# Kernel tuning notes

Measured on AMD Instinct MI355X. Metric: run time of the kernel, lower is better.

## Reference

```python
import jax, jax.numpy as jnp
import numpy as np
from jax import lax

DN = ('NHWC', 'HWIO', 'NHWC')
N_MEM = 2000  # memory slots
BN_EPS = 1e-3


def _conv(x, w, b):
    # tf.nn.conv2d stride 2, SAME, NHWC / HWIO
    return lax.conv_general_dilated(x, w, (2, 2), 'SAME', dimension_numbers=DN) + b


def _convt(x, w, b):
    # tf.nn.conv2d_transpose; w is TF layout [kh, kw, out_ch, in_ch]
    return lax.conv_transpose(x, w, (2, 2), 'SAME', dimension_numbers=DN,
                              transpose_kernel=True) + b


def _bn(x, g, b):
    # BatchNormalization(training=True): batch statistics over N,H,W
    m = jnp.mean(x, axis=(0, 1, 2))
    v = jnp.var(x, axis=(0, 1, 2))
    return g * (x - m) * lax.rsqrt(v + BN_EPS) + b


def setup_inputs() -> dict:
    key = jax.random.key(0)
    ks = iter(jax.random.split(key, 40))
    def gn(shape, s=0.05):
        return jax.random.normal(next(ks), shape, jnp.float32) * s
    inp = {'x': jax.random.uniform(next(ks), (16, 256, 256, 3), jnp.float32)}
    inp.update(
        w_e1=gn((1, 1, 3, 16)), b_e1=gn((16,)),
        g_bn1=jnp.ones(16, jnp.float32), be_bn1=jnp.zeros(16, jnp.float32),
        w_e2=gn((3, 3, 16, 32)), b_e2=gn((32,)),
        g_bn2=jnp.ones(32, jnp.float32), be_bn2=jnp.zeros(32, jnp.float32),
        w_e3=gn((3, 3, 32, 64)), b_e3=gn((64,)),
        g_bn3=jnp.ones(64, jnp.float32), be_bn3=jnp.zeros(64, jnp.float32),
        w_mem=gn((1, 1, N_MEM, 64)),
        w_d1=gn((3, 3, 32, 64)), b_d1=gn((32,)),
        g_bnt1=jnp.ones(32, jnp.float32), be_bnt1=jnp.zeros(32, jnp.float32),
        w_d2=gn((3, 3, 16, 32)), b_d2=gn((16,)),
        g_bnt2=jnp.ones(16, jnp.float32), be_bnt2=jnp.zeros(16, jnp.float32),
        w_d3=gn((3, 3, 3, 16)), b_d3=gn((3,)),
    )
    return inp


def reference(x, w_e1, b_e1, g_bn1, be_bn1, w_e2, b_e2, g_bn2, be_bn2,
              w_e3, b_e3, g_bn3, be_bn3, w_mem,
              w_d1, b_d1, g_bnt1, be_bnt1, w_d2, b_d2, g_bnt2, be_bnt2,
              w_d3, b_d3):
    # ---- encode ----
    h = jax.nn.relu(_bn(_conv(x, w_e1, b_e1), g_bn1, be_bn1))   # [B,128,128,16]
    h = jax.nn.relu(_bn(_conv(h, w_e2, b_e2), g_bn2, be_bn2))   # [B,64,64,32]
    z = jax.nn.relu(_bn(_conv(h, w_e3, b_e3), g_bn3, be_bn3))   # [B,32,32,64]
    # ---- memory addressing ----
    mem = w_mem[0, 0]                                            # [N, 64]
    num = jnp.einsum('bhwc,nc->bhwn', z, mem)
    den = jnp.einsum('bhwc,nc->bhwn', z * z, mem * mem)
    att = jax.nn.softmax((num + 1e-12) / (den + 1e-12), axis=-1)  # [B,32,32,N]
    d = att - 1.0 / N_MEM                                        # hard shrinkage
    renorm = jnp.clip(jax.nn.relu(d) * att / (jnp.abs(d) + 1e-12),
                      1e-12, 1.0 - 1e-12)
    z_hat = jnp.einsum('bhwn,nc->bhwc', renorm, mem)             # [B,32,32,64]
    # ---- decode ----
    t = jax.nn.relu(_bn(_convt(z_hat, w_d1, b_d1), g_bnt1, be_bnt1))  # [B,64,64,32]
    t = jax.nn.relu(_bn(_convt(t, w_d2, b_d2), g_bnt2, be_bnt2))      # [B,128,128,16]
    x_hat = jnp.clip(_convt(t, w_d3, b_d3), 1e-12, 1.0 - 1e-12)       # [B,256,256,3]
    return x_hat
```

## Files before the change

kernel.cpp:

```cpp
#include <hip/hip_runtime.h>
#include <math.h>

typedef __bf16 bf16x8 __attribute__((ext_vector_type(8)));
typedef __bf16 bf16x4 __attribute__((ext_vector_type(4)));
typedef float  f32x16 __attribute__((ext_vector_type(16)));

static __device__ __forceinline__ f32x16 zero16() {
  f32x16 v;
  #pragma unroll
  for (int i = 0; i < 16; ++i) v[i] = 0.f;
  return v;
}
static __device__ __forceinline__ unsigned int bfbits(__bf16 b) {
  return (unsigned int)__builtin_bit_cast(unsigned short, b);
}
static __device__ __forceinline__ bf16x8 mk8(unsigned int a, unsigned int b,
                                             unsigned int c, unsigned int d) {
  uint4 t; t.x = a; t.y = b; t.z = c; t.w = d;
  return __builtin_bit_cast(bf16x8, t);
}

__global__ __launch_bounds__(256) void k_conv1(const float* __restrict__ x,
    const float* __restrict__ w, const float* __restrict__ b, float* __restrict__ y,
    float* __restrict__ partials) {
  int t = blockIdx.x*256 + threadIdx.x;
  int ox = t & 127, oy = (t >> 7) & 127, bb = t >> 14;
  const float* xp = x + ((size_t)((bb*256 + 2*oy)*256 + 2*ox))*3;
  float x0 = xp[0], x1 = xp[1], x2 = xp[2];
  float4 rg[4];
  float4* yp = (float4*)(y + (size_t)t*16);
  #pragma unroll
  for (int g = 0; g < 4; ++g) {
    float4 r;
    r.x = b[g*4+0] + x0*w[g*4+0] + x1*w[16+g*4+0] + x2*w[32+g*4+0];
    r.y = b[g*4+1] + x0*w[g*4+1] + x1*w[16+g*4+1] + x2*w[32+g*4+1];
    r.z = b[g*4+2] + x0*w[g*4+2] + x1*w[16+g*4+2] + x2*w[32+g*4+2];
    r.w = b[g*4+3] + x0*w[g*4+3] + x1*w[16+g*4+3] + x2*w[32+g*4+3];
    rg[g] = r;
    yp[g] = r;
  }
  float4 s4[4], q4[4];
  #pragma unroll
  for (int g=0; g<4; ++g) {
    s4[g] = rg[g];
    q4[g] = make_float4(rg[g].x*rg[g].x, rg[g].y*rg[g].y, rg[g].z*rg[g].z, rg[g].w*rg[g].w);
  }
  #pragma unroll
  for (int off=1; off<64; off<<=1) {
    #pragma unroll
    for (int g=0; g<4; ++g) {
      s4[g].x += __shfl_xor(s4[g].x, off); s4[g].y += __shfl_xor(s4[g].y, off);
      s4[g].z += __shfl_xor(s4[g].z, off); s4[g].w += __shfl_xor(s4[g].w, off);
      q4[g].x += __shfl_xor(q4[g].x, off); q4[g].y += __shfl_xor(q4[g].y, off);
      q4[g].z += __shfl_xor(q4[g].z, off); q4[g].w += __shfl_xor(q4[g].w, off);
    }
  }
  __shared__ float red[4][32];
  int wv = threadIdx.x >> 6, lane = threadIdx.x & 63;
  if (lane == 0) {
    #pragma unroll
    for (int g=0; g<4; ++g) {
      *(float4*)&red[wv][g*4]      = s4[g];
      *(float4*)&red[wv][16 + g*4] = q4[g];
    }
  }
  __syncthreads();
  if (threadIdx.x < 32)
    partials[(size_t)blockIdx.x*32 + threadIdx.x] =
      red[0][threadIdx.x]+red[1][threadIdx.x]+red[2][threadIdx.x]+red[3][threadIdx.x];
}

template<int C,int CSPLIT>
__global__ __launch_bounds__(256) void k_finalize2(const float* __restrict__ partials, int nblk,
    double inv_n, const float* __restrict__ g, const float* __restrict__ be, float* __restrict__ ss) {
  const int COUTT = C/CSPLIT;
  const int NSTAT = 2*C;
  const int PER = 256/NSTAT;
  __shared__ double red[256];
  int tid = threadIdx.x;
  int st = tid % NSTAT, sub = tid / NSTAT;
  int c = st % C, kind = st / C;
  int cq = c / COUTT, j = c % COUTT;
  int nb = nblk / CSPLIT;
  double acc = 0.0;
  #pragma unroll 4
  for (int i = sub; i < nb; i += PER) {
    int bq = cq + i*CSPLIT;
    acc += (double)partials[(size_t)bq*2*COUTT + kind*COUTT + j];
  }
  red[tid] = acc;
  __syncthreads();
  for (int off = PER>>1; off > 0; off >>= 1) {
    if (sub < off) red[tid] += red[tid + off*NSTAT];
    __syncthreads();
  }
  if (tid < C) {
    double mean = red[tid]*inv_n;
    double var  = red[C+tid]*inv_n - mean*mean;
    float scale = g[tid] * rsqrtf((float)var + 1e-3f);
    float shift = be[tid] - (float)mean*scale;
    ss[tid] = scale; ss[C+tid] = shift;
  }
}

template<int CIN,int COUT,int CSPLIT,int HIN,int HOUT,bool BN>
__global__ __launch_bounds__(256) void k_conv_bn(const float* __restrict__ in,
    const float* __restrict__ w, const float* __restrict__ bias,
    const float* __restrict__ ss, float* __restrict__ y, float* __restrict__ partials) {
  const int COUTT = COUT/CSPLIT;
  const int NW4 = COUTT/4;
  __shared__ float4 wlds[9*CIN*NW4];
  int bid = blockIdx.x;
  int cq  = bid % CSPLIT;
  int pxb = bid / CSPLIT;
  int c0  = cq*COUTT;
  for (int e = threadIdx.x; e < 9*CIN*NW4; e += 256) {
    int r = e / NW4, cg = e % NW4;
    wlds[e] = *(const float4*)(w + (size_t)r*COUT + c0 + cg*4);
  }
  __syncthreads();
  int t0 = pxb*256 + threadIdx.x;
  float4 acc[NW4];
  #pragma unroll
  for (int g=0; g<NW4; ++g) acc[g] = *(const float4*)(bias + c0 + g*4);
  int ox = t0 % HOUT, oy = (t0/HOUT) % HOUT, bb = t0/(HOUT*HOUT);
  #pragma unroll 1
  for (int dy=0; dy<3; ++dy) {
    #pragma unroll 1
    for (int dx=0; dx<3; ++dx) {
      int tap = dy*3+dx;
      int iy = 2*oy + dy, ix = 2*ox + dx;
      if (iy < HIN && ix < HIN) {
        const float* bp = in + ((size_t)(bb*HIN + iy)*HIN + ix)*CIN;
        #pragma unroll
        for (int ci4=0; ci4<CIN/4; ++ci4) {
          float4 v = *(const float4*)(bp + ci4*4);
          if (BN) {
            float4 sc = *(const float4*)(ss + ci4*4);
            float4 sh = *(const float4*)(ss + CIN + ci4*4);
            v.x = fmaxf(0.f, fmaf(v.x, sc.x, sh.x));
            v.y = fmaxf(0.f, fmaf(v.y, sc.y, sh.y));
            v.z = fmaxf(0.f, fmaf(v.z, sc.z, sh.z));
            v.w = fmaxf(0.f, fmaf(v.w, sc.w, sh.w));
          }
          float va[4] = {v.x, v.y, v.z, v.w};
          #pragma unroll
          for (int k=0;k<4;++k) {
            float vk = va[k];
            #pragma unroll
            for (int g=0; g<NW4; ++g) {
              float4 w4 = wlds[(tap*CIN + ci4*4 + k)*NW4 + g];
              acc[g].x = fmaf(vk, w4.x, acc[g].x);
              acc[g].y = fmaf(vk, w4.y, acc[g].y);
              acc[g].z = fmaf(vk, w4.z, acc[g].z);
              acc[g].w = fmaf(vk, w4.w, acc[g].w);
            }
          }
        }
      }
    }
  }
  float4* yp = (float4*)(y + (size_t)t0*COUT + c0);
  #pragma unroll
  for (int g=0;g<NW4;++g) yp[g] = acc[g];
  float4 s4[NW4], q4[NW4];
  #pragma unroll
  for (int g=0; g<NW4; ++g) {
    s4[g] = acc[g];
    q4[g] = make_float4(acc[g].x*acc[g].x, acc[g].y*acc[g].y,
                        acc[g].z*acc[g].z, acc[g].w*acc[g].w);
  }
  #pragma unroll
  for (int off=1; off<64; off<<=1) {
    #pragma unroll
    for (int g=0; g<NW4; ++g) {
      s4[g].x += __shfl_xor(s4[g].x, off); s4[g].y += __shfl_xor(s4[g].y, off);
      s4[g].z += __shfl_xor(s4[g].z, off); s4[g].w += __shfl_xor(s4[g].w, off);
      q4[g].x += __shfl_xor(q4[g].x, off); q4[g].y += __shfl_xor(q4[g].y, off);
      q4[g].z += __shfl_xor(q4[g].z, off); q4[g].w += __shfl_xor(q4[g].w, off);
    }
  }
  __shared__ float red[4][2*COUTT];
  int wv = threadIdx.x >> 6, lane = threadIdx.x & 63;
  if (lane == 0) {
    #pragma unroll
    for (int g=0; g<NW4; ++g) {
      *(float4*)&red[wv][g*4]         = s4[g];
      *(float4*)&red[wv][COUTT + g*4] = q4[g];
    }
  }
  __syncthreads();
  if (threadIdx.x < 2*COUTT)
    partials[(size_t)bid*2*COUTT + threadIdx.x] =
      red[0][threadIdx.x]+red[1][threadIdx.x]+red[2][threadIdx.x]+red[3][threadIdx.x];
}


__global__ __launch_bounds__(256) void k_prep_z(const float* __restrict__ y3,
    const float* __restrict__ ss,
    __bf16* __restrict__ ZH, __bf16* __restrict__ ZL,
    __bf16* __restrict__ Z2H, __bf16* __restrict__ Z2L) {
  int t = blockIdx.x*256 + threadIdx.x;
  float4 v = ((const float4*)y3)[t];
  int c0 = (t*4) & 63;
  float4 sc = *(const float4*)(ss + c0);
  float4 sh = *(const float4*)(ss + 64 + c0);
  float vv[4];
  vv[0] = fmaxf(0.f, fmaf(v.x, sc.x, sh.x));
  vv[1] = fmaxf(0.f, fmaf(v.y, sc.y, sh.y));
  vv[2] = fmaxf(0.f, fmaf(v.z, sc.z, sh.z));
  vv[3] = fmaxf(0.f, fmaf(v.w, sc.w, sh.w));
  bf16x4 h, l, h2, l2;
  #pragma unroll
  for (int i=0;i<4;++i) {
    float f = vv[i];
    __bf16 hb = (__bf16)f;
    h[i] = hb; l[i] = (__bf16)(f - (float)hb);
    float q = f*f;
    __bf16 qb = (__bf16)q;
    h2[i] = qb; l2[i] = (__bf16)(q - (float)qb);
  }
  ((bf16x4*)ZH)[t] = h;  ((bf16x4*)ZL)[t] = l;
  ((bf16x4*)Z2H)[t] = h2; ((bf16x4*)Z2L)[t] = l2;
}

__global__ __launch_bounds__(256) void k_prep_m(const float* __restrict__ mem,
    __bf16* __restrict__ MH, __bf16* __restrict__ ML,
    __bf16* __restrict__ M2H, __bf16* __restrict__ M2L,
    __bf16* __restrict__ MHT, __bf16* __restrict__ MLT) {
  int t = blockIdx.x*256 + threadIdx.x;
  int n = t >> 4, c0 = (t & 15)*4;
  float4 v = make_float4(0.f,0.f,0.f,0.f);
  if (n < 2000) v = *(const float4*)(mem + (size_t)n*64 + c0);
  float vv[4] = {v.x, v.y, v.z, v.w};
  bf16x4 h, l, h2, l2;
  #pragma unroll
  for (int i=0;i<4;++i) {
    float f = vv[i];
    __bf16 hb = (__bf16)f;
    h[i] = hb; l[i] = (__bf16)(f - (float)hb);
    float q = f*f;
    __bf16 qb = (__bf16)q;
    h2[i] = qb; l2[i] = (__bf16)(q - (float)qb);
  }
  *(bf16x4*)(MH  + (size_t)n*64 + c0) = h;
  *(bf16x4*)(ML  + (size_t)n*64 + c0) = l;
  *(bf16x4*)(M2H + (size_t)n*64 + c0) = h2;
  *(bf16x4*)(M2L + (size_t)n*64 + c0) = l2;
  #pragma unroll
  for (int i=0;i<4;++i) {
    MHT[(size_t)(c0+i)*2048 + n] = h[i];
    MLT[(size_t)(c0+i)*2048 + n] = l[i];
  }
}

__global__ __launch_bounds__(64) void k_pass1(
    const __bf16* __restrict__ ZH, const __bf16* __restrict__ ZL,
    const __bf16* __restrict__ Z2H, const __bf16* __restrict__ Z2L,
    const __bf16* __restrict__ MH, const __bf16* __restrict__ ML,
    const __bf16* __restrict__ M2H, const __bf16* __restrict__ M2L,
    __bf16* __restrict__ U, float* __restrict__ MT,
    float* __restrict__ partM, float* __restrict__ partS) {
  int pb = blockIdx.x & 511, chunk = blockIdx.x >> 9;
  int lane = threadIdx.x;
  int p0 = pb*32;
  int col = lane & 31, hi = lane >> 5;
  bf16x8 bzh[4], bzl[4], b2h[4], b2l[4];
  size_t zoff = (size_t)(p0 + col)*64 + hi*8;
  #pragma unroll
  for (int ks=0;ks<4;++ks) {
    bzh[ks] = *(const bf16x8*)(ZH  + zoff + ks*16);
    bzl[ks] = *(const bf16x8*)(ZL  + zoff + ks*16);
    b2h[ks] = *(const bf16x8*)(Z2H + zoff + ks*16);
    b2l[ks] = *(const bf16x8*)(Z2L + zoff + ks*16);
  }
  float m = -3.4e38f, S = 0.f;
  int nbase = chunk*256;
  #pragma unroll 2
  for (int t=0; t<8; ++t) {
    int n0 = nbase + t*32;
    size_t arow = (size_t)(n0 + col)*64 + hi*8;
    f32x16 num = zero16(), den = zero16();
    #pragma unroll
    for (int ks=0;ks<4;++ks) {
      bf16x8 amh = *(const bf16x8*)(MH + arow + ks*16);
      bf16x8 aml = *(const bf16x8*)(ML + arow + ks*16);
      num = __builtin_amdgcn_mfma_f32_32x32x16_bf16(amh, bzh[ks], num, 0,0,0);
      num = __builtin_amdgcn_mfma_f32_32x32x16_bf16(amh, bzl[ks], num, 0,0,0);
      num = __builtin_amdgcn_mfma_f32_32x32x16_bf16(aml, bzh[ks], num, 0,0,0);
      bf16x8 a2h = *(const bf16x8*)(M2H + arow + ks*16);
      bf16x8 a2l = *(const bf16x8*)(M2L + arow + ks*16);
      den = __builtin_amdgcn_mfma_f32_32x32x16_bf16(a2h, b2h[ks], den, 0,0,0);
      den = __builtin_amdgcn_mfma_f32_32x32x16_bf16(a2h, b2l[ks], den, 0,0,0);
      den = __builtin_amdgcn_mfma_f32_32x32x16_bf16(a2l, b2h[ks], den, 0,0,0);
    }
    bool maskt = (n0 + 32 > 2000);
    float sv[16];
    float tmax = -3.4e38f;
    #pragma unroll
    for (int r=0;r<16;++r) {
      float s = (num[r] + 1e-12f) * __builtin_amdgcn_rcpf(den[r] + 1e-12f);
      if (maskt) {
        int nn = n0 + (r&3) + 8*(r>>2) + 4*hi;
        if (nn >= 2000) s = -3.4e38f;
      }
      sv[r] = s;
      tmax = fmaxf(tmax, s);
    }
    float mn = fmaxf(m, tmax);
    float ssum = 0.f;
    unsigned int up[8];
    #pragma unroll
    for (int j=0;j<8;++j) {
      float u0 = __expf(sv[2*j]   - mn);
      float u1 = __expf(sv[2*j+1] - mn);
      ssum += u0; ssum += u1;
      up[j] = bfbits((__bf16)u0) | (bfbits((__bf16)u1) << 16);
    }
    S = S*__expf(m - mn) + ssum;
    m = mn;
    size_t idx = (size_t)((chunk*8 + t)*16384 + p0 + col)*2 + hi;
    uint4 st0; st0.x = up[0]; st0.y = up[1]; st0.z = up[2]; st0.w = up[3];
    uint4 st1; st1.x = up[4]; st1.y = up[5]; st1.z = up[6]; st1.w = up[7];
    *(uint4*)(U + idx*16)     = st0;
    *(uint4*)(U + idx*16 + 8) = st1;
    MT[idx] = mn;
  }
  float mo = __shfl_xor(m, 32);
  float So = __shfl_xor(S, 32);
  float mf = fmaxf(m, mo);
  float Sf = S*__expf(m - mf) + So*__expf(mo - mf);
  if (lane < 32) {
    int p = p0 + col;
    partM[chunk*16384 + p] = mf;
    partS[chunk*16384 + p] = Sf;
  }
}

__global__ __launch_bounds__(64) void k_pass2(
    const __bf16* __restrict__ U, const float* __restrict__ MT,
    const __bf16* __restrict__ MHT, const __bf16* __restrict__ MLT,
    const float* __restrict__ partM, const float* __restrict__ partS,
    float* __restrict__ ZP) {
  int pb = blockIdx.x & 511, chunk = blockIdx.x >> 9;
  int lane = threadIdx.x;
  int p0 = pb*32;
  int col = lane & 31, hi = lane >> 5;
  int p = p0 + col;
  float pmv[8];
  float Mp = -3.4e38f;
  #pragma unroll
  for (int c=0;c<8;++c) { pmv[c] = partM[c*16384 + p]; Mp = fmaxf(Mp, pmv[c]); }
  float Ssum = 0.f;
  #pragma unroll
  for (int c=0;c<8;++c) Ssum += partS[c*16384 + p] * __expf(pmv[c] - Mp);
  float CM  = Mp + __logf(Ssum);
  float thr = CM - 7.6009025f;
  f32x16 za0 = zero16(), za1 = zero16();
  int nbase = chunk*256;
  #pragma unroll 2
  for (int t=0; t<8; ++t) {
    int n0 = nbase + t*32;
    size_t idx = (size_t)((chunk*8 + t)*16384 + p)*2 + hi;
    uint4 a = *(const uint4*)(U + idx*16);
    uint4 b = *(const uint4*)(U + idx*16 + 8);
    float mt = MT[idx];
    float scale = __expf(mt - CM);
    float thru  = __expf(thr - mt);
    unsigned int ua[8] = {a.x,a.y,a.z,a.w,b.x,b.y,b.z,b.w};
    unsigned int qh[8];
    #pragma unroll
    for (int j=0;j<8;++j) {
      float u0 = __builtin_bit_cast(float, ua[j] << 16);
      float u1 = __builtin_bit_cast(float, ua[j] & 0xffff0000u);
      float r0 = (u0 > thru) ? u0*scale : 0.f;
      float r1 = (u1 > thru) ? u1*scale : 0.f;
      qh[j] = bfbits((__bf16)r0) | (bfbits((__bf16)r1) << 16);
    }
    unsigned int qhp[8];
    #pragma unroll
    for (int i=0;i<8;++i) qhp[i] = (unsigned int)__shfl_xor((int)qh[i], 32);
    bf16x8 f1h = hi ? mk8(qhp[2],qhp[3],qh[2],qh[3]) : mk8(qh[0],qh[1],qhp[0],qhp[1]);
    bf16x8 f2h = hi ? mk8(qhp[6],qhp[7],qh[6],qh[7]) : mk8(qh[4],qh[5],qhp[4],qhp[5]);
    #pragma unroll
    for (int kh=0; kh<2; ++kh) {
      bf16x8 fh = kh ? f2h : f1h;
      size_t bofs = (size_t)col*2048 + n0 + kh*16 + hi*8;
      bf16x8 bmh0 = *(const bf16x8*)(MHT + bofs);
      bf16x8 bml0 = *(const bf16x8*)(MLT + bofs);
      bf16x8 bmh1 = *(const bf16x8*)(MHT + bofs + (size_t)32*2048);
      bf16x8 bml1 = *(const bf16x8*)(MLT + bofs + (size_t)32*2048);
      za0 = __builtin_amdgcn_mfma_f32_32x32x16_bf16(fh, bmh0, za0, 0,0,0);
      za0 = __builtin_amdgcn_mfma_f32_32x32x16_bf16(fh, bml0, za0, 0,0,0);
      za1 = __builtin_amdgcn_mfma_f32_32x32x16_bf16(fh, bmh1, za1, 0,0,0);
      za1 = __builtin_amdgcn_mfma_f32_32x32x16_bf16(fh, bml1, za1, 0,0,0);
    }
  }
  size_t base = (size_t)chunk << 20;
  #pragma unroll
  for (int r=0;r<16;++r) {
    int prow = (r&3) + 8*(r>>2) + 4*hi;
    size_t o = base + (size_t)(p0 + prow)*64 + col;
    ZP[o]      = za0[r];
    ZP[o + 32] = za1[r];
  }
}

__global__ __launch_bounds__(256) void k_zcomb(const float* __restrict__ ZP,
                                               float* __restrict__ Gz) {
  int t = blockIdx.x*256 + threadIdx.x;
  float a = 0.f;
  #pragma unroll
  for (int c=0;c<8;++c) a += ZP[(size_t)c*1048576 + t];
  Gz[t] = a;
}

template<int CIN,int COUT,int CSPLIT,int HIN,bool BN>
__global__ __launch_bounds__(256) void k_convt_bn(const float* __restrict__ in,
    const float* __restrict__ w, const float* __restrict__ bias,
    const float* __restrict__ ss, float* __restrict__ y, float* __restrict__ partials) {
  const int COUTT = COUT/CSPLIT;
  const int HOUT = 2*HIN;
  __shared__ float4 wlds[4*COUTT*(CIN/4)];
  int bid = blockIdx.x;
  int cq = bid % CSPLIT; int rest = bid / CSPLIT;
  int cls = rest % 4;    int pxb = rest / 4;
  int pm = cls >> 1, pn = cls & 1;
  int c0 = cq*COUTT;
  int NTI = (pm == 0) ? 2 : 1;
  int NTJ = (pn == 0) ? 2 : 1;
  int NT = NTI*NTJ;
  for (int e = threadIdx.x; e < NT*COUTT*(CIN/4); e += 256) {
    int tl = e / (COUTT*(CIN/4));
    int rem = e % (COUTT*(CIN/4));
    int cc = rem / (CIN/4), ci4 = rem % (CIN/4);
    int ki = pm + 2*(tl / NTJ), kj = pn + 2*(tl % NTJ);
    wlds[e] = *(const float4*)(w + ((size_t)(ki*3+kj)*COUT + c0 + cc)*CIN + ci4*4);
  }
  __syncthreads();
  int t0 = pxb*256 + threadIdx.x;
  float acc[COUTT];
  #pragma unroll
  for (int cc=0;cc<COUTT;++cc) acc[cc] = bias[c0+cc];
  int nx = t0 % HIN, my = (t0/HIN) % HIN, bb = t0/(HIN*HIN);
  #pragma unroll 1
  for (int ti=0; ti<NTI; ++ti) {
    #pragma unroll 1
    for (int tj=0; tj<NTJ; ++tj) {
      int tl = ti*NTJ + tj;
      int i = my - ti, j = nx - tj;
      if (i >= 0 && j >= 0) {
        const float* bp = in + ((size_t)(bb*HIN + i)*HIN + j)*CIN;
        #pragma unroll
        for (int ci4=0; ci4<CIN/4; ++ci4) {
          float4 v = *(const float4*)(bp + ci4*4);
          if (BN) {
            float4 sc = *(const float4*)(ss + ci4*4);
            float4 sh = *(const float4*)(ss + CIN + ci4*4);
            v.x = fmaxf(0.f, fmaf(v.x, sc.x, sh.x));
            v.y = fmaxf(0.f, fmaf(v.y, sc.y, sh.y));
            v.z = fmaxf(0.f, fmaf(v.z, sc.z, sh.z));
            v.w = fmaxf(0.f, fmaf(v.w, sc.w, sh.w));
          }
          #pragma unroll
          for (int cc=0;cc<COUTT;++cc) {
            float4 w4 = wlds[(tl*COUTT + cc)*(CIN/4) + ci4];
            float a = acc[cc];
            a = fmaf(v.x, w4.x, a);
            a = fmaf(v.y, w4.y, a);
            a = fmaf(v.z, w4.z, a);
            a = fmaf(v.w, w4.w, a);
            acc[cc] = a;
          }
        }
      }
    }
  }
  int m = 2*my + pm, n = 2*nx + pn;
  float* yp = y + ((size_t)(bb*HOUT + m)*HOUT + n)*COUT + c0;
  #pragma unroll
  for (int g=0;g<COUTT/4;++g)
    ((float4*)yp)[g] = make_float4(acc[g*4], acc[g*4+1], acc[g*4+2], acc[g*4+3]);
  float s[COUTT], q[COUTT];
  #pragma unroll
  for (int cc=0;cc<COUTT;++cc) { s[cc] = acc[cc]; q[cc] = acc[cc]*acc[cc]; }
  #pragma unroll
  for (int off=1; off<64; off<<=1) {
    #pragma unroll
    for (int cc=0;cc<COUTT;++cc) {
      s[cc] += __shfl_xor(s[cc], off);
      q[cc] += __shfl_xor(q[cc], off);
    }
  }
  __shared__ float red[4][2*COUTT];
  int wv = threadIdx.x >> 6, lane = threadIdx.x & 63;
  if (lane == 0) {
    #pragma unroll
    for (int cc=0;cc<COUTT;++cc) { red[wv][cc] = s[cc]; red[wv][COUTT+cc] = q[cc]; }
  }
  __syncthreads();
  if (threadIdx.x < 2*COUTT)
    partials[(size_t)bid*2*COUTT + threadIdx.x] =
      red[0][threadIdx.x]+red[1][threadIdx.x]+red[2][threadIdx.x]+red[3][threadIdx.x];
}

__global__ __launch_bounds__(256) void k_convt_final(const float* __restrict__ in,
    const float* __restrict__ w, const float* __restrict__ bias,
    const float* __restrict__ ss, float* __restrict__ out) {
  const int CIN=16, HIN=128, HOUT=256;
  __shared__ float4 wlds[4*3*4];
  int cls = blockIdx.x & 3;
  int pxb = blockIdx.x >> 2;
  int pm = cls >> 1, pn = cls & 1;
  int NTI = (pm == 0) ? 2 : 1;
  int NTJ = (pn == 0) ? 2 : 1;
  int NT = NTI*NTJ;
  if (threadIdx.x < NT*3*4) {
    int e = threadIdx.x;
    int tl = e / 12, rem = e % 12;
    int c = rem / 4, ci4 = rem % 4;
    int ki = pm + 2*(tl / NTJ), kj = pn + 2*(tl % NTJ);
    wlds[e] = *(const float4*)(w + ((size_t)(ki*3+kj)*3 + c)*CIN + ci4*4);
  }
  __syncthreads();
  int t = pxb*256 + threadIdx.x;
  int nx = t % HIN, my = (t/HIN) % HIN, bb = t/(HIN*HIN);
  float a0 = bias[0], a1 = bias[1], a2 = bias[2];
  #pragma unroll 1
  for (int ti=0; ti<NTI; ++ti) {
    #pragma unroll 1
    for (int tj=0; tj<NTJ; ++tj) {
      int tl = ti*NTJ + tj;
      int i = my - ti, j = nx - tj;
      if (i >= 0 && j >= 0) {
        const float* bp = in + ((size_t)(bb*HIN + i)*HIN + j)*CIN;
        #pragma unroll
        for (int ci4=0; ci4<4; ++ci4) {
          float4 v = *(const float4*)(bp + ci4*4);
          float4 sc = *(const float4*)(ss + ci4*4);
          float4 sh = *(const float4*)(ss + CIN + ci4*4);
          v.x = fmaxf(0.f, fmaf(v.x, sc.x, sh.x));
          v.y = fmaxf(0.f, fmaf(v.y, sc.y, sh.y));
          v.z = fmaxf(0.f, fmaf(v.z, sc.z, sh.z));
          v.w = fmaxf(0.f, fmaf(v.w, sc.w, sh.w));
          float4 w0 = wlds[(tl*3 + 0)*4 + ci4];
          float4 w1 = wlds[(tl*3 + 1)*4 + ci4];
          float4 w2 = wlds[(tl*3 + 2)*4 + ci4];
          a0 = fmaf(v.x, w0.x, a0); a0 = fmaf(v.y, w0.y, a0);
          a0 = fmaf(v.z, w0.z, a0); a0 = fmaf(v.w, w0.w, a0);
          a1 = fmaf(v.x, w1.x, a1); a1 = fmaf(v.y, w1.y, a1);
          a1 = fmaf(v.z, w1.z, a1); a1 = fmaf(v.w, w1.w, a1);
          a2 = fmaf(v.x, w2.x, a2); a2 = fmaf(v.y, w2.y, a2);
          a2 = fmaf(v.z, w2.z, a2); a2 = fmaf(v.w, w2.w, a2);
        }
      }
    }
  }
  int m = 2*my + pm, n = 2*nx + pn;
  float* op = out + ((size_t)(bb*HOUT + m)*HOUT + n)*3;
  op[0] = fminf(fmaxf(a0, 1e-12f), 1.0f);
  op[1] = fminf(fmaxf(a1, 1e-12f), 1.0f);
  op[2] = fminf(fmaxf(a2, 1e-12f), 1.0f);
}

extern "C" void kernel_launch(void* const* d_in, const int* in_sizes, int n_in,
                              void* d_out, int out_size, void* d_ws, size_t ws_size,
                              hipStream_t stream) {
  const float* x    = (const float*)d_in[0];
  const float* w_e1 = (const float*)d_in[1];
  const float* b_e1 = (const float*)d_in[2];
  const float* g1   = (const float*)d_in[3];
  const float* be1  = (const float*)d_in[4];
  const float* w_e2 = (const float*)d_in[5];
  const float* b_e2 = (const float*)d_in[6];
  const float* g2   = (const float*)d_in[7];
  const float* be2  = (const float*)d_in[8];
  const float* w_e3 = (const float*)d_in[9];
  const float* b_e3 = (const float*)d_in[10];
  const float* g3   = (const float*)d_in[11];
  const float* be3  = (const float*)d_in[12];
  const float* wmem = (const float*)d_in[13];
  const float* w_d1 = (const float*)d_in[14];
  const float* b_d1 = (const float*)d_in[15];
  const float* gt1  = (const float*)d_in[16];
  const float* bet1 = (const float*)d_in[17];
  const float* w_d2 = (const float*)d_in[18];
  const float* b_d2 = (const float*)d_in[19];
  const float* gt2  = (const float*)d_in[20];
  const float* bet2 = (const float*)d_in[21];
  const float* w_d3 = (const float*)d_in[22];
  const float* b_d3 = (const float*)d_in[23];
  float* out = (float*)d_out;

  float* ws = (float*)d_ws;
  __bf16* U  = (__bf16*)ws;
  float* A   = ws;
  float* Cc  = ws + 4194304;
  float* Gz  = ws + 16777216;
  float* ZP  = Gz + 1048576;
  float* E   = ZP + 8388608;
  float* bfbase = E + 1048576;
  __bf16* ZH  = (__bf16*)bfbase;
  __bf16* ZL  = ZH  + 16384*64;
  __bf16* Z2H = ZL  + 16384*64;
  __bf16* Z2L = Z2H + 16384*64;
  __bf16* MH  = Z2L + 16384*64;
  __bf16* ML  = MH  + 2048*64;
  __bf16* M2H = ML  + 2048*64;
  __bf16* M2L = M2H + 2048*64;
  __bf16* MHT = M2L + 2048*64;
  __bf16* MLT = MHT + 64*2048;
  float* PT   = (float*)(MLT + 64*2048);
  float* SS   = PT + 131072;
  float* PM   = SS + 256;
  float* PS   = PM + 131072;
  float* MT   = PS + 131072;
  (void)ws_size; (void)in_sizes; (void)n_in; (void)out_size;

  k_conv1<<<1024,256,0,stream>>>(x, w_e1, b_e1, A, PT);
  k_finalize2<16,1><<<1,256,0,stream>>>(PT, 1024, 1.0/262144.0, g1, be1, SS);
  k_conv_bn<16,32,2,128,64,true><<<512,256,0,stream>>>(A, w_e2, b_e2, SS, Cc, PT);
  k_finalize2<32,2><<<1,256,0,stream>>>(PT, 512, 1.0/65536.0, g2, be2, SS);
  k_conv_bn<32,64,8,64,32,true><<<512,256,0,stream>>>(Cc, w_e3, b_e3, SS, E, PT);
  k_finalize2<64,8><<<1,256,0,stream>>>(PT, 512, 1.0/16384.0, g3, be3, SS);
  k_prep_m<<<128,256,0,stream>>>(wmem, MH, ML, M2H, M2L, MHT, MLT);
  k_prep_z<<<1024,256,0,stream>>>(E, SS, ZH, ZL, Z2H, Z2L);
  k_pass1<<<4096,64,0,stream>>>(ZH, ZL, Z2H, Z2L, MH, ML, M2H, M2L, U, MT, PM, PS);
  k_pass2<<<4096,64,0,stream>>>(U, MT, MHT, MLT, PM, PS, ZP);
  k_zcomb<<<4096,256,0,stream>>>(ZP, Gz);
  k_convt_bn<64,32,2,32,false><<<512,256,0,stream>>>(Gz, w_d1, b_d1, nullptr, Cc, PT);
  k_finalize2<32,2><<<1,256,0,stream>>>(PT, 512, 1.0/65536.0, gt1, bet1, SS);
  k_convt_bn<32,16,1,64,true><<<1024,256,0,stream>>>(Cc, w_d2, b_d2, SS, A, PT);
  k_finalize2<16,1><<<1,256,0,stream>>>(PT, 1024, 1.0/262144.0, gt2, bet2, SS);
  k_convt_final<<<4096,256,0,stream>>>(A, w_d3, b_d3, SS, out);
}
```

Measured before the change: 362.8 us.

## Split softmax pass1 into 16 chunks, reorder blocks, store pass2 partials as bf16

Pass1 now splits the memory dimension into 16 chunks of 128 slots each, giving twice as many blocks. Each 32-slot tile keeps its own local max, and the tiles are merged at the end rather than through a running rescale, which removes the serial dependence between tiles. Block indexing now puts the chunk in the low bits, so blocks covering the same pixel tile run next to each other for better cache reuse. Pass2 reads 16 partial max/sum pairs and writes its per-chunk z partials in bf16, halving that write and the later read in zcomb, at the cost of some precision in the summed output.

```diff
diff --git a/kernel.cpp b/kernel.cpp
--- a/kernel.cpp
+++ b/kernel.cpp
@@ -261,7 +261,7 @@
     const __bf16* __restrict__ M2H, const __bf16* __restrict__ M2L,
     __bf16* __restrict__ U, float* __restrict__ MT,
     float* __restrict__ partM, float* __restrict__ partS) {
-  int pb = blockIdx.x & 511, chunk = blockIdx.x >> 9;
+  int chunk = blockIdx.x & 15, pb = blockIdx.x >> 4;
   int lane = threadIdx.x;
   int p0 = pb*32;
   int col = lane & 31, hi = lane >> 5;
@@ -274,10 +274,10 @@
     b2h[ks] = *(const bf16x8*)(Z2H + zoff + ks*16);
     b2l[ks] = *(const bf16x8*)(Z2L + zoff + ks*16);
   }
-  float m = -3.4e38f, S = 0.f;
-  int nbase = chunk*256;
-  #pragma unroll 2
-  for (int t=0; t<8; ++t) {
+  float tmaxv[4], ssumv[4];
+  int nbase = chunk*128;
+  #pragma unroll
+  for (int t=0; t<4; ++t) {
     int n0 = nbase + t*32;
     size_t arow = (size_t)(n0 + col)*64 + hi*8;
     f32x16 num = zero16(), den = zero16();
@@ -307,25 +307,26 @@
       sv[r] = s;
       tmax = fmaxf(tmax, s);
     }
-    float mn = fmaxf(m, tmax);
     float ssum = 0.f;
     unsigned int up[8];
     #pragma unroll
     for (int j=0;j<8;++j) {
-      float u0 = __expf(sv[2*j]   - mn);
-      float u1 = __expf(sv[2*j+1] - mn);
+      float u0 = __expf(sv[2*j]   - tmax);
+      float u1 = __expf(sv[2*j+1] - tmax);
       ssum += u0; ssum += u1;
       up[j] = bfbits((__bf16)u0) | (bfbits((__bf16)u1) << 16);
     }
-    S = S*__expf(m - mn) + ssum;
-    m = mn;
-    size_t idx = (size_t)((chunk*8 + t)*16384 + p0 + col)*2 + hi;
+    size_t idx = (size_t)((chunk*4 + t)*16384 + p0 + col)*2 + hi;
     uint4 st0; st0.x = up[0]; st0.y = up[1]; st0.z = up[2]; st0.w = up[3];
     uint4 st1; st1.x = up[4]; st1.y = up[5]; st1.z = up[6]; st1.w = up[7];
     *(uint4*)(U + idx*16)     = st0;
     *(uint4*)(U + idx*16 + 8) = st1;
-    MT[idx] = mn;
-  }
+    MT[idx] = tmax;
+    tmaxv[t] = tmax; ssumv[t] = ssum;
+  }
+  float m = fmaxf(fmaxf(tmaxv[0], tmaxv[1]), fmaxf(tmaxv[2], tmaxv[3]));
+  float S = ssumv[0]*__expf(tmaxv[0]-m) + ssumv[1]*__expf(tmaxv[1]-m)
+          + ssumv[2]*__expf(tmaxv[2]-m) + ssumv[3]*__expf(tmaxv[3]-m);
   float mo = __shfl_xor(m, 32);
   float So = __shfl_xor(S, 32);
   float mf = fmaxf(m, mo);
@@ -341,19 +342,19 @@
     const __bf16* __restrict__ U, const float* __restrict__ MT,
     const __bf16* __restrict__ MHT, const __bf16* __restrict__ MLT,
     const float* __restrict__ partM, const float* __restrict__ partS,
-    float* __restrict__ ZP) {
-  int pb = blockIdx.x & 511, chunk = blockIdx.x >> 9;
+    __bf16* __restrict__ ZPb) {
+  int chunk = blockIdx.x & 7, pb = blockIdx.x >> 3;
   int lane = threadIdx.x;
   int p0 = pb*32;
   int col = lane & 31, hi = lane >> 5;
   int p = p0 + col;
-  float pmv[8];
+  float pmv[16];
   float Mp = -3.4e38f;
   #pragma unroll
-  for (int c=0;c<8;++c) { pmv[c] = partM[c*16384 + p]; Mp = fmaxf(Mp, pmv[c]); }
+  for (int c=0;c<16;++c) { pmv[c] = partM[c*16384 + p]; Mp = fmaxf(Mp, pmv[c]); }
   float Ssum = 0.f;
   #pragma unroll
-  for (int c=0;c<8;++c) Ssum += partS[c*16384 + p] * __expf(pmv[c] - Mp);
+  for (int c=0;c<16;++c) Ssum += partS[c*16384 + p] * __expf(pmv[c] - Mp);
   float CM  = Mp + __logf(Ssum);
   float thr = CM - 7.6009025f;
   f32x16 za0 = zero16(), za1 = zero16();
@@ -401,17 +402,17 @@
   for (int r=0;r<16;++r) {
     int prow = (r&3) + 8*(r>>2) + 4*hi;
     size_t o = base + (size_t)(p0 + prow)*64 + col;
-    ZP[o]      = za0[r];
-    ZP[o + 32] = za1[r];
-  }
-}
-
-__global__ __launch_bounds__(256) void k_zcomb(const float* __restrict__ ZP,
+    ZPb[o]      = (__bf16)za0[r];
+    ZPb[o + 32] = (__bf16)za1[r];
+  }
+}
+
+__global__ __launch_bounds__(256) void k_zcomb(const __bf16* __restrict__ ZPb,
                                                float* __restrict__ Gz) {
   int t = blockIdx.x*256 + threadIdx.x;
   float a = 0.f;
   #pragma unroll
-  for (int c=0;c<8;++c) a += ZP[(size_t)c*1048576 + t];
+  for (int c=0;c<8;++c) a += (float)ZPb[(size_t)c*1048576 + t];
   Gz[t] = a;
 }
 
@@ -597,8 +598,8 @@
   float* A   = ws;
   float* Cc  = ws + 4194304;
   float* Gz  = ws + 16777216;
-  float* ZP  = Gz + 1048576;
-  float* E   = ZP + 8388608;
+  __bf16* ZPb = (__bf16*)(Gz + 1048576);
+  float* E   = Gz + 1048576 + 8388608;
   float* bfbase = E + 1048576;
   __bf16* ZH  = (__bf16*)bfbase;
   __bf16* ZL  = ZH  + 16384*64;
@@ -613,8 +614,8 @@
   float* PT   = (float*)(MLT + 64*2048);
   float* SS   = PT + 131072;
   float* PM   = SS + 256;
-  float* PS   = PM + 131072;
-  float* MT   = PS + 131072;
+  float* PS   = PM + 262144;
+  float* MT   = PS + 262144;
   (void)ws_size; (void)in_sizes; (void)n_in; (void)out_size;
 
   k_conv1<<<1024,256,0,stream>>>(x, w_e1, b_e1, A, PT);
@@ -625,9 +626,9 @@
   k_finalize2<64,8><<<1,256,0,stream>>>(PT, 512, 1.0/16384.0, g3, be3, SS);
   k_prep_m<<<128,256,0,stream>>>(wmem, MH, ML, M2H, M2L, MHT, MLT);
   k_prep_z<<<1024,256,0,stream>>>(E, SS, ZH, ZL, Z2H, Z2L);
-  k_pass1<<<4096,64,0,stream>>>(ZH, ZL, Z2H, Z2L, MH, ML, M2H, M2L, U, MT, PM, PS);
-  k_pass2<<<4096,64,0,stream>>>(U, MT, MHT, MLT, PM, PS, ZP);
-  k_zcomb<<<4096,256,0,stream>>>(ZP, Gz);
+  k_pass1<<<8192,64,0,stream>>>(ZH, ZL, Z2H, Z2L, MH, ML, M2H, M2L, U, MT, PM, PS);
+  k_pass2<<<4096,64,0,stream>>>(U, MT, MHT, MLT, PM, PS, ZPb);
+  k_zcomb<<<4096,256,0,stream>>>(ZPb, Gz);
   k_convt_bn<64,32,2,32,false><<<512,256,0,stream>>>(Gz, w_d1, b_d1, nullptr, Cc, PT);
   k_finalize2<32,2><<<1,256,0,stream>>>(PT, 512, 1.0/65536.0, gt1, bet1, SS);
   k_convt_bn<32,16,1,64,true><<<1024,256,0,stream>>>(Cc, w_d2, b_d2, SS, A, PT);
```

After: 358.8 us. No clear change (-1.1%).
